# Kernel optimization log

Hardware: AMD Instinct MI355X
Metric: run time of the kernel (lower is better)

The kernel has to match this reference:

```python
import jax, jax.numpy as jnp
import numpy as np
import math

N, C, W, H = 8, 1024, 1024, 16
D = C // H  # head size = 64


def setup_inputs() -> dict:
    key = jax.random.key(0)
    ks = jax.random.split(key, 7)
    s = 1.0 / math.sqrt(C)
    return {
        "hidden_states": jax.random.normal(ks[0], (N, C, W), jnp.float32),
        "attention_mask": jnp.zeros((N, 1, 1, W), jnp.float32),
        "wq": jax.random.normal(ks[1], (C, C), jnp.float32) * s,
        "bq": jax.random.normal(ks[2], (C,), jnp.float32) * 0.02,
        "wk": jax.random.normal(ks[3], (C, C), jnp.float32) * s,
        "bk": jax.random.normal(ks[4], (C,), jnp.float32) * 0.02,
        "wv": jax.random.normal(ks[5], (C, C), jnp.float32) * s,
        "bv": jax.random.normal(ks[6], (C,), jnp.float32) * 0.02,
    }


def reference(hidden_states, attention_mask, wq, bq, wk, bk, wv, bv):
    # conv1d(kernel=1, groups=1) == per-position GEMM: [N,C,W] x [Cout,Cin] -> [N,Cout,W]
    q = jnp.einsum('ncw,oc->now', hidden_states, wq) + bq[None, :, None]
    k = jnp.einsum('ncw,oc->now', hidden_states, wk) + bk[None, :, None]
    v = jnp.einsum('ncw,oc->now', hidden_states, wv) + bv[None, :, None]
    # split heads: [N,C,W] -> [N,H,D,W]
    q = q.reshape(N, H, D, W).transpose(0, 1, 3, 2)  # [N,H,W,D]
    k = k.reshape(N, H, D, W)                         # [N,H,D,W]
    v = v.reshape(N, H, D, W).transpose(0, 1, 3, 2)  # [N,H,W,D]
    scores = jnp.einsum('nhqd,nhdk->nhqk', q, k) / math.sqrt(D)
    scores = scores + attention_mask  # broadcast [N,1,1,W]
    probs = jax.nn.softmax(scores, axis=-1)
    ctx = jnp.einsum('nhqk,nhkd->nhqd', probs, v)    # [N,H,W,D]
    # merge heads back to [N,C,W]
    return ctx.transpose(0, 1, 3, 2).reshape(N, C, W)
```

## Files before the change

### kernel.cpp

```cpp
#include <hip/hip_runtime.h>
#include <hip/hip_bf16.h>

typedef __bf16 bf16x8 __attribute__((ext_vector_type(8)));
typedef __bf16 bf16x4 __attribute__((ext_vector_type(4)));
typedef float f32x4 __attribute__((ext_vector_type(4)));

#define N_ 8
#define C_ 1024
#define W_ 1024
#define H_ 16
#define D_ 64

typedef __attribute__((address_space(3))) void lds_void;
typedef const __attribute__((address_space(1))) void gbl_void;
static __device__ __forceinline__ void gload_lds16(const void* g, void* l) {
    __builtin_amdgcn_global_load_lds((gbl_void*)g, (lds_void*)l, 16, 0, 0);
}

__global__ __launch_bounds__(256)
void convert_w(const float* __restrict__ s0, const float* __restrict__ s1,
               const float* __restrict__ s2, __bf16* __restrict__ dst) {
    const float* s = blockIdx.y == 0 ? s0 : (blockIdx.y == 1 ? s1 : s2);
    __bf16* d = dst + (long)blockIdx.y * C_ * C_;
    const long i = ((long)blockIdx.x * 256 + threadIdx.x) * 8;
    f32x4 a = *(const f32x4*)(const void*)(s + i);
    f32x4 b = *(const f32x4*)(const void*)(s + i + 4);
    bf16x8 v;
    #pragma unroll
    for (int t = 0; t < 4; ++t) { v[t] = (__bf16)a[t]; v[t + 4] = (__bf16)b[t]; }
    *(bf16x8*)(void*)(d + i) = v;
}

__global__ __launch_bounds__(256)
void transpose_x(const float* __restrict__ in, __bf16* __restrict__ outp) {
    __shared__ float tile[64][68];
    const long bin  = (long)blockIdx.z * C_ * W_;
    const long bout = (long)blockIdx.z * W_ * C_;
    const int w0 = blockIdx.x * 64, c0 = blockIdx.y * 64;
    const int t = threadIdx.x;
    const int rr = t >> 4;
    const int cg = (t & 15) * 4;
    #pragma unroll
    for (int it = 0; it < 4; ++it) {
        const int cr = it * 16 + rr;
        f32x4 v = *(const f32x4*)(const void*)(in + bin + (long)(c0 + cr) * W_ + w0 + cg);
        *(f32x4*)&tile[cr][cg] = v;
    }
    __syncthreads();
    #pragma unroll
    for (int it = 0; it < 4; ++it) {
        const int wr = it * 16 + rr;
        bf16x4 o;
        #pragma unroll
        for (int u = 0; u < 4; ++u) o[u] = (__bf16)tile[cg + u][wr];
        *(bf16x4*)(void*)(outp + bout + (long)(w0 + wr) * C_ + c0 + cg) = o;
    }
}

template<int OUT_T>
static __device__ __forceinline__
void gemm_body(const __bf16* __restrict__ Aw, const __bf16* __restrict__ Xn,
               const float* __restrict__ bias, __bf16* __restrict__ Pn,
               const int o0, const int w0,
               __bf16* __restrict__ As, __bf16* __restrict__ Bs) {
    constexpr int BK = 64;
    const int tid = threadIdx.x;
    const int wv = tid >> 6, lane = tid & 63;
    const int l15 = lane & 15, quad = lane >> 4;
    const int wr = (wv >> 1) * 64, wc = (wv & 1) * 64;
    const int lr8 = lane >> 3;
    const int lp = lane & 7;

    f32x4 acc[4][4] = {};

    for (int k0 = 0; k0 < C_; k0 += BK) {
        #pragma unroll
        for (int j = 0; j < 4; ++j) {
            const int seg = wv * 4 + j;
            const int r = seg * 8 + lr8;
            const int q = lp ^ (r & 7);
            gload_lds16(Aw + (long)(o0 + r) * C_ + k0 + q * 8, As + seg * 512);
            gload_lds16(Xn + (long)(w0 + r) * C_ + k0 + q * 8, Bs + seg * 512);
        }
        __syncthreads();
        bf16x8 af[4][2], bf[4][2];
        #pragma unroll
        for (int mt = 0; mt < 4; ++mt) {
            const int R = wr + mt * 16 + l15;
            #pragma unroll
            for (int s = 0; s < 2; ++s) {
                const int pos = (s * 4 + quad) ^ (R & 7);
                af[mt][s] = *(const bf16x8*)(const void*)&As[R * 64 + pos * 8];
            }
        }
        #pragma unroll
        for (int nt = 0; nt < 4; ++nt) {
            const int R = wc + nt * 16 + l15;
            #pragma unroll
            for (int s = 0; s < 2; ++s) {
                const int pos = (s * 4 + quad) ^ (R & 7);
                bf[nt][s] = *(const bf16x8*)(const void*)&Bs[R * 64 + pos * 8];
            }
        }
        #pragma unroll
        for (int s = 0; s < 2; ++s)
            #pragma unroll
            for (int mt = 0; mt < 4; ++mt)
                #pragma unroll
                for (int nt = 0; nt < 4; ++nt) {
                    if (OUT_T == 0)
                        acc[mt][nt] = __builtin_amdgcn_mfma_f32_16x16x32_bf16(af[mt][s], bf[nt][s], acc[mt][nt], 0, 0, 0);
                    else
                        acc[mt][nt] = __builtin_amdgcn_mfma_f32_16x16x32_bf16(bf[nt][s], af[mt][s], acc[mt][nt], 0, 0, 0);
                }
        __syncthreads();
    }

    #pragma unroll
    for (int mt = 0; mt < 4; ++mt) {
        #pragma unroll
        for (int nt = 0; nt < 4; ++nt) {
            #pragma unroll
            for (int rg = 0; rg < 4; ++rg) {
                if (OUT_T == 0) {
                    const int col = w0 + wc + nt * 16 + l15;
                    const int row = o0 + wr + mt * 16 + quad * 4 + rg;
                    Pn[(long)row * W_ + col] = (__bf16)(acc[mt][nt][rg] + bias[row]);
                } else {
                    const int o = o0 + wr + mt * 16 + l15;
                    const int w = w0 + wc + nt * 16 + quad * 4 + rg;
                    Pn[(long)w * C_ + o] = (__bf16)(acc[mt][nt][rg] + bias[o]);
                }
            }
        }
    }
}

__global__ __launch_bounds__(256)
void gemm_qkv(const __bf16* __restrict__ Wb, const __bf16* __restrict__ Xt,
              const float* __restrict__ bq, const float* __restrict__ bk,
              const float* __restrict__ bv,
              __bf16* __restrict__ Qt, __bf16* __restrict__ Kt,
              __bf16* __restrict__ Vb) {
    __shared__ __align__(16) __bf16 As[128 * 64];
    __shared__ __align__(16) __bf16 Bs[128 * 64];
    const int f = blockIdx.x;
    const int n = f & 7;
    const int j = f >> 3;
    const int which = j >> 6;
    const int t = j & 63;
    const int o0 = (t >> 3) * 128;
    const int w0 = (t & 7) * 128;
    const size_t SZ = (size_t)C_ * W_;
    const size_t WSZ = (size_t)C_ * C_;
    const __bf16* Xn = Xt + (size_t)n * SZ;
    const __bf16* Aw = Wb + (size_t)which * WSZ;
    if (which < 2)
        gemm_body<1>(Aw, Xn, which ? bk : bq, (which ? Kt : Qt) + n * SZ, o0, w0, As, Bs);
    else
        gemm_body<0>(Aw, Xn, bv, Vb + n * SZ, o0, w0, As, Bs);
}

__global__ __launch_bounds__(256)
void flash_attn(const __bf16* __restrict__ Qt,
                const __bf16* __restrict__ Kt,
                const __bf16* __restrict__ V,
                const float* __restrict__ mask,
                float* __restrict__ out) {
    __shared__ __align__(16) __bf16 Pl[4 * 16 * 64];
    __shared__ __align__(16) __bf16 Ks[2][64 * 64];
    __shared__ __align__(16) __bf16 Vs[2][64 * 64];

    const int f = blockIdx.x;
    const int g = (f & 7) + ((f >> 6) << 3);
    const int m = (f >> 3) & 7;
    const int n = g >> 4, h = g & 15;
    const int q0 = m * 128;

    const int tid = threadIdx.x;
    const int wave = tid >> 6, lane = tid & 63;
    const int l15 = lane & 15, quad = lane >> 4;
    const int lr8 = lane >> 3, lp = lane & 7;
    const long nqk = (long)n * W_ * C_;
    const long nv = (long)n * C_ * W_;
    const int hD = h * D_;
    const float* mrow = mask + (long)n * W_;
    constexpr float SC = 0.125f * 1.44269504f;
    constexpr float L2E = 1.44269504f;

    char* plb = (char*)Pl + wave * 2048;
    const int swz = (l15 & 7) << 4;
    const long plrow = l15 * 128;

    bf16x8 aq[2][2];
    #pragma unroll
    for (int qs = 0; qs < 2; ++qs)
        #pragma unroll
        for (int dc = 0; dc < 2; ++dc)
            aq[qs][dc] = *(const bf16x8*)(const void*)
                (Qt + nqk + (long)(q0 + wave * 32 + qs * 16 + l15) * C_ + hD + dc * 32 + quad * 8);

    f32x4 o_acc[2][4] = {};
    float l_ln[2] = {};

    auto stage = [&](int kt, int b) {
        #pragma unroll
        for (int jj = 0; jj < 2; ++jj) {
            const int seg = wave * 2 + jj;
            const int r = seg * 8 + lr8;
            const int q = lp ^ (r & 7);
            gload_lds16(Kt + nqk + (long)(kt + r) * C_ + hD + q * 8, &Ks[b][seg * 512]);
            gload_lds16(V + nv + (long)(hD + r) * W_ + kt + q * 8, &Vs[b][seg * 512]);
        }
    };

    stage(0, 0);

    for (int ti = 0; ti < W_ / 64; ++ti) {
        const int kt = ti * 64;
        const int cur = ti & 1;
        asm volatile("s_waitcnt vmcnt(0)" ::: "memory");
        __syncthreads();
        if (ti + 1 < W_ / 64) stage(kt + 64, cur ^ 1);

        bf16x8 bk[4][2], bv[4][2];
        #pragma unroll
        for (int ks = 0; ks < 4; ++ks)
            #pragma unroll
            for (int dc = 0; dc < 2; ++dc) {
                const int R = ks * 16 + l15;
                const int pos = (dc * 4 + quad) ^ (R & 7);
                bk[ks][dc] = *(const bf16x8*)(const void*)&Ks[cur][R * 64 + pos * 8];
            }
        #pragma unroll
        for (int ds = 0; ds < 4; ++ds)
            #pragma unroll
            for (int kc = 0; kc < 2; ++kc) {
                const int R = ds * 16 + l15;
                const int pos = (kc * 4 + quad) ^ (R & 7);
                bv[ds][kc] = *(const bf16x8*)(const void*)&Vs[cur][R * 64 + pos * 8];
            }
        f32x4 mk[4];
        #pragma unroll
        for (int ks = 0; ks < 4; ++ks)
            mk[ks] = *(const f32x4*)(const void*)(mrow + kt + ks * 16 + quad * 4);

        #pragma unroll
        for (int qs = 0; qs < 2; ++qs) {
            f32x4 s[4] = {};
            #pragma unroll
            for (int ks = 0; ks < 4; ++ks)
                #pragma unroll
                for (int dc = 0; dc < 2; ++dc)
                    s[ks] = __builtin_amdgcn_mfma_f32_16x16x32_bf16(bk[ks][dc], aq[qs][dc], s[ks], 0, 0, 0);
            #pragma unroll
            for (int ks = 0; ks < 4; ++ks) {
                #pragma unroll
                for (int rg = 0; rg < 4; ++rg)
                    s[ks][rg] = __builtin_exp2f(s[ks][rg] * SC + mk[ks][rg] * L2E);
                l_ln[qs] += (s[ks][0] + s[ks][1]) + (s[ks][2] + s[ks][3]);
            }
            #pragma unroll
            for (int ks = 0; ks < 4; ++ks) {
                bf16x4 p4;
                #pragma unroll
                for (int rg = 0; rg < 4; ++rg) p4[rg] = (__bf16)s[ks][rg];
                *(bf16x4*)(void*)(plb + plrow + (((ks * 32 + quad * 8) ^ swz))) = p4;
            }
            bf16x8 ap[2];
            #pragma unroll
            for (int kc = 0; kc < 2; ++kc)
                ap[kc] = *(const bf16x8*)(const void*)(plb + plrow + (((kc * 64 + quad * 16) ^ swz)));
            #pragma unroll
            for (int ds = 0; ds < 4; ++ds)
                #pragma unroll
                for (int kc = 0; kc < 2; ++kc)
                    o_acc[qs][ds] = __builtin_amdgcn_mfma_f32_16x16x32_bf16(ap[kc], bv[ds][kc], o_acc[qs][ds], 0, 0, 0);
        }
    }

    #pragma unroll
    for (int qs = 0; qs < 2; ++qs) {
        float l = l_ln[qs];
        l += __shfl_xor(l, 16, 64);
        l += __shfl_xor(l, 32, 64);
        const float linv = 1.0f / l;
        #pragma unroll
        for (int rg = 0; rg < 4; ++rg) {
            const float inv = __shfl(linv, quad * 4 + rg, 64);
            #pragma unroll
            for (int ds = 0; ds < 4; ++ds)
                out[nv + (long)(hD + ds * 16 + l15) * W_ + q0 + wave * 32 + qs * 16 + quad * 4 + rg]
                    = o_acc[qs][ds][rg] * inv;
        }
    }
}

extern "C" void kernel_launch(void* const* d_in, const int* in_sizes, int n_in,
                              void* d_out, int out_size, void* d_ws, size_t ws_size,
                              hipStream_t stream) {
    (void)in_sizes; (void)n_in; (void)out_size; (void)ws_size;
    const float* hs   = (const float*)d_in[0];
    const float* mask = (const float*)d_in[1];
    const float* wq   = (const float*)d_in[2];
    const float* bq   = (const float*)d_in[3];
    const float* wk   = (const float*)d_in[4];
    const float* bk   = (const float*)d_in[5];
    const float* wv   = (const float*)d_in[6];
    const float* bv   = (const float*)d_in[7];
    float* out = (float*)d_out;

    const size_t SZ = (size_t)N_ * C_ * W_;
    const size_t WSZ = (size_t)C_ * C_;
    __bf16* Wb = (__bf16*)d_ws;
    __bf16* Xt = Wb + 3 * WSZ;
    __bf16* Qt = Xt + SZ;
    __bf16* Kt = Qt + SZ;
    __bf16* Vb = Kt + SZ;

    convert_w<<<dim3(512, 3), 256, 0, stream>>>(wq, wk, wv, Wb);
    transpose_x<<<dim3(W_ / 64, C_ / 64, N_), 256, 0, stream>>>(hs, Xt);

    gemm_qkv<<<dim3(1536), 256, 0, stream>>>(Wb, Xt, bq, bk, bv, Qt, Kt, Vb);

    flash_attn<<<dim3(1024), 256, 0, stream>>>(Qt, Kt, Vb, mask, out);
}
```

Baseline: 248.7 us.

## Load K/V tiles straight from global into registers, dropping LDS staging

The attention kernel no longer stages K and V tiles through double-buffered LDS with barriers. Each wave now loads its MFMA operands directly from global memory (relying on L2 reuse across the four waves) and keeps only a per-wave P scratch buffer, enlarged to hold both query sub-tiles. It also splits the loop into a score phase and a PV phase, uses raw exp2 with a pre-scaled mask, raises MFMA priority with setprio, and sets launch bounds to 4 blocks per CU. The aim is to remove barrier and LDS overhead and raise occupancy, at the risk of redundant global/L2 traffic and exposed load latency without software prefetch.

New measurement: 295.5 us. 1.19x slower.

```diff
diff --git a/kernel.cpp b/kernel.cpp
--- a/kernel.cpp
+++ b/kernel.cpp
@@ -161,15 +161,13 @@
         gemm_body<0>(Aw, Xn, bv, Vb + n * SZ, o0, w0, As, Bs);
 }
 
-__global__ __launch_bounds__(256)
+__global__ __launch_bounds__(256, 4)
 void flash_attn(const __bf16* __restrict__ Qt,
                 const __bf16* __restrict__ Kt,
                 const __bf16* __restrict__ V,
                 const float* __restrict__ mask,
                 float* __restrict__ out) {
-    __shared__ __align__(16) __bf16 Pl[4 * 16 * 64];
-    __shared__ __align__(16) __bf16 Ks[2][64 * 64];
-    __shared__ __align__(16) __bf16 Vs[2][64 * 64];
+    __shared__ __align__(16) __bf16 Pl[4 * 2 * 16 * 64];
 
     const int f = blockIdx.x;
     const int g = (f & 7) + ((f >> 6) << 3);
@@ -180,7 +178,6 @@
     const int tid = threadIdx.x;
     const int wave = tid >> 6, lane = tid & 63;
     const int l15 = lane & 15, quad = lane >> 4;
-    const int lr8 = lane >> 3, lp = lane & 7;
     const long nqk = (long)n * W_ * C_;
     const long nv = (long)n * C_ * W_;
     const int hD = h * D_;
@@ -188,9 +185,12 @@
     constexpr float SC = 0.125f * 1.44269504f;
     constexpr float L2E = 1.44269504f;
 
-    char* plb = (char*)Pl + wave * 2048;
+    char* plb = (char*)Pl + wave * 4096;
     const int swz = (l15 & 7) << 4;
-    const long plrow = l15 * 128;
+    const int plrow = l15 * 128;
+
+    const __bf16* kp = Kt + nqk + (long)l15 * C_ + hD + quad * 8;
+    const __bf16* vp = V + nv + (long)(hD + l15) * W_ + quad * 8;
 
     bf16x8 aq[2][2];
     #pragma unroll
@@ -203,61 +203,40 @@
     f32x4 o_acc[2][4] = {};
     float l_ln[2] = {};
 
-    auto stage = [&](int kt, int b) {
-        #pragma unroll
-        for (int jj = 0; jj < 2; ++jj) {
-            const int seg = wave * 2 + jj;
-            const int r = seg * 8 + lr8;
-            const int q = lp ^ (r & 7);
-            gload_lds16(Kt + nqk + (long)(kt + r) * C_ + hD + q * 8, &Ks[b][seg * 512]);
-            gload_lds16(V + nv + (long)(hD + r) * W_ + kt + q * 8, &Vs[b][seg * 512]);
-        }
-    };
-
-    stage(0, 0);
-
+    #pragma unroll 1
     for (int ti = 0; ti < W_ / 64; ++ti) {
         const int kt = ti * 64;
-        const int cur = ti & 1;
-        asm volatile("s_waitcnt vmcnt(0)" ::: "memory");
-        __syncthreads();
-        if (ti + 1 < W_ / 64) stage(kt + 64, cur ^ 1);
-
-        bf16x8 bk[4][2], bv[4][2];
+
+        bf16x8 bk[4][2];
         #pragma unroll
         for (int ks = 0; ks < 4; ++ks)
             #pragma unroll
-            for (int dc = 0; dc < 2; ++dc) {
-                const int R = ks * 16 + l15;
-                const int pos = (dc * 4 + quad) ^ (R & 7);
-                bk[ks][dc] = *(const bf16x8*)(const void*)&Ks[cur][R * 64 + pos * 8];
-            }
-        #pragma unroll
-        for (int ds = 0; ds < 4; ++ds)
-            #pragma unroll
-            for (int kc = 0; kc < 2; ++kc) {
-                const int R = ds * 16 + l15;
-                const int pos = (kc * 4 + quad) ^ (R & 7);
-                bv[ds][kc] = *(const bf16x8*)(const void*)&Vs[cur][R * 64 + pos * 8];
-            }
-        f32x4 mk[4];
-        #pragma unroll
-        for (int ks = 0; ks < 4; ++ks)
-            mk[ks] = *(const f32x4*)(const void*)(mrow + kt + ks * 16 + quad * 4);
+            for (int dc = 0; dc < 2; ++dc)
+                bk[ks][dc] = *(const bf16x8*)(const void*)
+                    (kp + (long)(kt + ks * 16) * C_ + dc * 32);
+        f32x4 mk2[4];
+        #pragma unroll
+        for (int ks = 0; ks < 4; ++ks) {
+            f32x4 mv = *(const f32x4*)(const void*)(mrow + kt + ks * 16 + quad * 4);
+            #pragma unroll
+            for (int rg = 0; rg < 4; ++rg) mk2[ks][rg] = mv[rg] * L2E;
+        }
 
         #pragma unroll
         for (int qs = 0; qs < 2; ++qs) {
             f32x4 s[4] = {};
+            __builtin_amdgcn_s_setprio(1);
             #pragma unroll
             for (int ks = 0; ks < 4; ++ks)
                 #pragma unroll
                 for (int dc = 0; dc < 2; ++dc)
                     s[ks] = __builtin_amdgcn_mfma_f32_16x16x32_bf16(bk[ks][dc], aq[qs][dc], s[ks], 0, 0, 0);
+            __builtin_amdgcn_s_setprio(0);
             #pragma unroll
             for (int ks = 0; ks < 4; ++ks) {
                 #pragma unroll
                 for (int rg = 0; rg < 4; ++rg)
-                    s[ks][rg] = __builtin_exp2f(s[ks][rg] * SC + mk[ks][rg] * L2E);
+                    s[ks][rg] = __builtin_amdgcn_exp2f(s[ks][rg] * SC + mk2[ks][rg]);
                 l_ln[qs] += (s[ks][0] + s[ks][1]) + (s[ks][2] + s[ks][3]);
             }
             #pragma unroll
@@ -265,17 +244,32 @@
                 bf16x4 p4;
                 #pragma unroll
                 for (int rg = 0; rg < 4; ++rg) p4[rg] = (__bf16)s[ks][rg];
-                *(bf16x4*)(void*)(plb + plrow + (((ks * 32 + quad * 8) ^ swz))) = p4;
-            }
+                *(bf16x4*)(void*)(plb + qs * 2048 + plrow + ((ks * 32 + quad * 8) ^ swz)) = p4;
+            }
+        }
+
+        bf16x8 bv[4][2];
+        #pragma unroll
+        for (int ds = 0; ds < 4; ++ds)
+            #pragma unroll
+            for (int kc = 0; kc < 2; ++kc)
+                bv[ds][kc] = *(const bf16x8*)(const void*)
+                    (vp + (long)(ds * 16) * W_ + kt + kc * 32);
+
+        #pragma unroll
+        for (int qs = 0; qs < 2; ++qs) {
             bf16x8 ap[2];
             #pragma unroll
             for (int kc = 0; kc < 2; ++kc)
-                ap[kc] = *(const bf16x8*)(const void*)(plb + plrow + (((kc * 64 + quad * 16) ^ swz)));
+                ap[kc] = *(const bf16x8*)(const void*)
+                    (plb + qs * 2048 + plrow + ((kc * 64 + quad * 16) ^ swz));
+            __builtin_amdgcn_s_setprio(1);
             #pragma unroll
             for (int ds = 0; ds < 4; ++ds)
                 #pragma unroll
                 for (int kc = 0; kc < 2; ++kc)
                     o_acc[qs][ds] = __builtin_amdgcn_mfma_f32_16x16x32_bf16(ap[kc], bv[ds][kc], o_acc[qs][ds], 0, 0, 0);
+            __builtin_amdgcn_s_setprio(0);
         }
     }
 
```
